# Kernel optimization log

Hardware: AMD Instinct MI355X
Metric: run time of the kernel (lower is better)

Reference implementation:

```python
import jax, jax.numpy as jnp
import numpy as np

N = 100000      # nodes
F_IN = 512      # num_features
H = 256         # hidden
C = 64          # num_classes
E = 3200000     # edges
K = 10          # APPNP propagation steps
ALPHA = 0.1     # teleport probability


def setup_inputs() -> dict:
    key = jax.random.key(0)
    k_x, k_w0, k_w1, k_e = jax.random.split(key, 4)
    x = jax.random.normal(k_x, (N, F_IN), dtype=jnp.float32)
    w0 = jax.random.normal(k_w0, (F_IN, H), dtype=jnp.float32) / np.sqrt(F_IN).astype(np.float32)
    b0 = jnp.zeros((H,), dtype=jnp.float32)
    w1 = jax.random.normal(k_w1, (H, C), dtype=jnp.float32) / np.sqrt(H).astype(np.float32)
    b1 = jnpps = jnp.zeros((C,), dtype=jnp.float32)
    edge_index = jax.random.randint(k_e, (2, E), 0, N, dtype=jnp.int64)
    return {"x": x, "w0": w0, "b0": b0, "w1": w1, "b1": b1, "edge_index": edge_index}


def _appnp(h, edge_index):
    # Add self loops (PyG APPNP default: gcn_norm with self loops).
    loops = jnp.arange(N, dtype=edge_index.dtype)
    src = jnp.concatenate([edge_index[0], loops])
    dst = jnp.concatenate([edge_index[1], loops])
    # Symmetric GCN normalization: D^{-1/2} (A+I) D^{-1/2}
    deg = jax.ops.segment_sum(jnp.ones_like(src, dtype=h.dtype), dst, num_segments=N)
    dinv = jnp.where(deg > 0, jax.lax.rsqrt(deg), 0.0)
    norm = dinv[src] * dinv[dst]  # [E+N]

    def step(xc, _):
        msg = norm[:, None] * xc[src]                      # gather [E+N, C]
        agg = jax.ops.segment_sum(msg, dst, num_segments=N)  # scatter-add [N, C]
        return (1.0 - ALPHA) * agg + ALPHA * h, None

    out, _ = jax.lax.scan(step, h, None, length=K)
    return out


def reference(x, w0, b0, w1, b1, edge_index):
    # eval mode: dropout is identity
    h = jax.nn.relu(x @ w0 + b0)   # [N, H]
    h = h @ w1 + b1                # [N, C]
    z = _appnp(h, edge_index)      # [N, C]
    return jax.nn.log_softmax(z, axis=1)
```

## Files before the change

kernel.cpp:

```cpp
#include <hip/hip_runtime.h>
#include <hip/hip_bf16.h>

#define NN 100000
#define EE 3200000
#define FIN 512
#define HH 256
#define CC 64
#define KSTEPS 10
#define SB 391
#define NBUC 782
#define EPB 16384
#define NEB 196

typedef __attribute__((ext_vector_type(8))) short bf16x8;
typedef __attribute__((ext_vector_type(8))) short s16x8;
typedef __attribute__((ext_vector_type(4))) float f32x4;
typedef unsigned short ushort_t;

__device__ __forceinline__ short f2bf(float f) {
    union { __hip_bfloat16 h; short s; } u;
    u.h = __float2bfloat16(f);
    return u.s;
}

__device__ __forceinline__ void glds16(const void* g, void* l) {
    __builtin_amdgcn_global_load_lds(
        (const __attribute__((address_space(1))) void*)g,
        (__attribute__((address_space(3))) void*)l, 16, 0, 0);
}

__global__ void prep_w(const float* __restrict__ w0, const float* __restrict__ w1,
                       short* __restrict__ w0t, short* __restrict__ w1t) {
    int t = blockIdx.x * blockDim.x + threadIdx.x;
    if (t < FIN * HH) {
        int k = t >> 8, n = t & 255;
        w0t[n * FIN + k] = f2bf(w0[t]);
    } else if (t < FIN * HH + HH * CC) {
        int u = t - FIN * HH;
        int k = u >> 6, n = u & 63;
        w1t[n * HH + k] = f2bf(w1[u]);
    }
}

__global__ __launch_bounds__(256) void x2b_kernel(const float* __restrict__ x,
                                                  ushort_t* __restrict__ xb) {
    const long NTOT = (long)NN * FIN;
    long stride = (long)gridDim.x * 256 * 8;
    for (long i = ((long)blockIdx.x * 256 + threadIdx.x) * 8; i < NTOT; i += stride) {
        float4 a = *(const float4*)(x + i);
        float4 b = *(const float4*)(x + i + 4);
        s16x8 o;
        o[0] = f2bf(a.x); o[1] = f2bf(a.y); o[2] = f2bf(a.z); o[3] = f2bf(a.w);
        o[4] = f2bf(b.x); o[5] = f2bf(b.y); o[6] = f2bf(b.z); o[7] = f2bf(b.w);
        *(s16x8*)(xb + i) = o;
    }
}

__global__ __launch_bounds__(256) void bincnt(const int* __restrict__ ei,
                                              int* __restrict__ bcnt) {
    __shared__ int hb[NBUC];
    int tid = threadIdx.x;
    int base = blockIdx.x * EPB;
    for (int i = tid; i < NBUC; i += 256) hb[i] = 0;
    __syncthreads();
#pragma unroll 4
    for (int i = 0; i < EPB / 256; ++i) {
        int t = base + i * 256 + tid;
        if (t < EE) atomicAdd(&hb[(unsigned)ei[EE + t] >> 7], 1);
    }
    __syncthreads();
    for (int i = tid; i < NBUC; i += 256)
        if (hb[i]) atomicAdd(&bcnt[i], hb[i]);
}

__global__ __launch_bounds__(1024) void bscan(const int* __restrict__ bcnt,
                                              int* __restrict__ eboff) {
    __shared__ int sh[1024];
    int t = threadIdx.x;
    int v = (t < NBUC) ? bcnt[t] : 0;
    sh[t] = v;
    __syncthreads();
    for (int off = 1; off < 1024; off <<= 1) {
        int add = (t >= off) ? sh[t - off] : 0;
        __syncthreads();
        sh[t] += add;
        __syncthreads();
    }
    if (t < NBUC) eboff[t] = sh[t] - v;
}

__global__ __launch_bounds__(256) void binfill(const int* __restrict__ ei,
                                               const int* __restrict__ eboff,
                                               int* __restrict__ bfc,
                                               int* __restrict__ stg) {
    __shared__ int hb[NBUC];
    __shared__ int lb[NBUC];
    int tid = threadIdx.x;
    int base = blockIdx.x * EPB;
    for (int i = tid; i < NBUC; i += 256) hb[i] = 0;
    __syncthreads();
#pragma unroll 4
    for (int i = 0; i < EPB / 256; ++i) {
        int t = base + i * 256 + tid;
        if (t < EE) atomicAdd(&hb[(unsigned)ei[EE + t] >> 7], 1);
    }
    __syncthreads();
    for (int i = tid; i < NBUC; i += 256) {
        int c = hb[i];
        lb[i] = eboff[i] + (c ? atomicAdd(&bfc[i], c) : 0);
        hb[i] = 0;
    }
    __syncthreads();
#pragma unroll 4
    for (int i = 0; i < EPB / 256; ++i) {
        int t = base + i * 256 + tid;
        if (t < EE) {
            int s = ei[t];
            int d = ei[EE + t];
            int b = (unsigned)d >> 7;
            int o = atomicAdd(&hb[b], 1);
            stg[lb[b] + o] = (s << 7) | (d & 127);
        }
    }
}

__global__ __launch_bounds__(256) void bhist(const int* __restrict__ stg,
                                             const int* __restrict__ eboff,
                                             const int* __restrict__ bcnt,
                                             int* __restrict__ cnt) {
    __shared__ int nc[128];
    int b = blockIdx.x, tid = threadIdx.x;
    if (tid < 128) nc[tid] = 0;
    __syncthreads();
    int s0 = eboff[b], n = bcnt[b];
    for (int i = tid; i < n; i += 256) atomicAdd(&nc[stg[s0 + i] & 127], 1);
    __syncthreads();
    int node = b * 128 + tid;
    if (tid < 128 && node < NN) cnt[node] = nc[tid];
}

__global__ __launch_bounds__(256) void deg_kernel(const int* __restrict__ cnt,
                                                  float* __restrict__ dinv,
                                                  float* __restrict__ wco,
                                                  float* __restrict__ sdg,
                                                  int* __restrict__ bsum,
                                                  int* __restrict__ dbc) {
    __shared__ int red[256];
    __shared__ int h[64];
    int tid = threadIdx.x;
    if (tid < 64) h[tid] = 0;
    int i = blockIdx.x * 256 + tid;
    int d = 0, bin = 0;
    if (i < NN) {
        int c = cnt[i];
        d = c + 1;
        bin = min(c, 63);
        float fd = (float)d;
        dinv[i] = rsqrtf(fd);
        wco[i] = 0.9f / fd;
        sdg[i] = sqrtf(fd);
    }
    red[tid] = d;
    __syncthreads();
    if (i < NN) atomicAdd(&h[bin], 1);
    for (int off = 128; off > 0; off >>= 1) {
        if (tid < off) red[tid] += red[tid + off];
        __syncthreads();
    }
    if (tid == 0) bsum[blockIdx.x] = red[0];
    if (tid < 64 && h[tid]) atomicAdd(&dbc[tid], h[tid]);
}

__global__ __launch_bounds__(512) void scanb_kernel(const int* __restrict__ bsum,
                                                    int* __restrict__ boff,
                                                    const int* __restrict__ dbc,
                                                    int* __restrict__ dboff) {
    __shared__ int sh[512];
    int t = threadIdx.x;
    int v = (t < SB) ? bsum[t] : 0;
    sh[t] = v;
    __syncthreads();
    for (int off = 1; off < 512; off <<= 1) {
        int add = (t >= off) ? sh[t - off] : 0;
        __syncthreads();
        sh[t] += add;
        __syncthreads();
    }
    if (t < SB) boff[t] = sh[t] - v;
    __syncthreads();
    int v2 = (t < 64) ? dbc[t] : 0;
    __syncthreads();
    if (t < 64) sh[t] = v2;
    __syncthreads();
    for (int off = 1; off < 64; off <<= 1) {
        int add = (t >= off && t < 64) ? sh[t - off] : 0;
        __syncthreads();
        if (t < 64) sh[t] += add;
        __syncthreads();
    }
    if (t < 64) dboff[t] = sh[t] - v2;
}

__global__ __launch_bounds__(256) void rp_kernel(const int* __restrict__ cnt,
                                                 const int* __restrict__ boff,
                                                 int* __restrict__ rp) {
    __shared__ int sh[256];
    int i = blockIdx.x * 256 + threadIdx.x;
    int d = (i < NN) ? cnt[i] + 1 : 0;
    sh[threadIdx.x] = d;
    __syncthreads();
    for (int off = 1; off < 256; off <<= 1) {
        int add = (threadIdx.x >= off) ? sh[threadIdx.x - off] : 0;
        __syncthreads();
        sh[threadIdx.x] += add;
        __syncthreads();
    }
    int incl = sh[threadIdx.x];
    if (i < NN) rp[i] = boff[blockIdx.x] + incl - d;
    if (i == NN - 1) rp[NN] = boff[blockIdx.x] + incl;
}

__global__ __launch_bounds__(256) void bfill2(const int* __restrict__ stg,
                                              const int* __restrict__ eboff,
                                              const int* __restrict__ bcnt,
                                              const int* __restrict__ rp,
                                              int* __restrict__ eds) {
    __shared__ int nfc[128];
    __shared__ int rpl[129];
    int b = blockIdx.x, tid = threadIdx.x;
    int nodes = min(128, NN - b * 128);
    if (tid < 128) nfc[tid] = 0;
    if (tid <= 128) rpl[tid] = rp[min(b * 128 + tid, NN)];
    __syncthreads();
    int s0 = eboff[b], n = bcnt[b];
    for (int i = tid; i < n; i += 256) {
        int e = stg[s0 + i];
        int loc = e & 127;
        int o = atomicAdd(&nfc[loc], 1);
        eds[rpl[loc] + o] = e >> 7;
    }
    __syncthreads();
    if (tid < nodes) eds[rpl[tid + 1] - 1] = b * 128 + tid;
}

__global__ __launch_bounds__(256) void dperm(const int* __restrict__ cnt,
                                             const int* __restrict__ dboff,
                                             int* __restrict__ dfc,
                                             int* __restrict__ perm) {
    __shared__ int h[64];
    __shared__ int base[64];
    int tid = threadIdx.x;
    int i = blockIdx.x * 256 + tid;
    if (tid < 64) h[tid] = 0;
    __syncthreads();
    int bin = 0, r = 0;
    bool ok = i < NN;
    if (ok) {
        bin = min(cnt[i], 63);
        r = atomicAdd(&h[bin], 1);
    }
    __syncthreads();
    if (tid < 64) {
        int c = h[tid];
        base[tid] = dboff[tid] + (c ? atomicAdd(&dfc[tid], c) : 0);
    }
    __syncthreads();
    if (ok) perm[base[bin] + r] = i;
}

__global__ __launch_bounds__(256) void gemm1(const ushort_t* __restrict__ xb,
                                             const short* __restrict__ w0t,
                                             const float* __restrict__ b0,
                                             short* __restrict__ h0) {
    __shared__ __align__(16) short As[2][128 * 64];
    __shared__ __align__(16) short Bs[2][128 * 64];
    const int tid = threadIdx.x;
    const int lane = tid & 63;
    const int wid = tid >> 6;
    const int wm = wid >> 1, wn = wid & 1;
    const int bn0 = blockIdx.x * 128;
    const long row0 = (long)blockIdx.y * 128;
    const int rl = lane >> 3;
    const int gko = (lane & 7) ^ rl;

    auto stage = [&](int kt, int buf) {
#pragma unroll
        for (int j = 0; j < 4; ++j) {
            int blk = wid * 4 + j;
            const ushort_t* g = xb + (row0 + blk * 8 + rl) * FIN + kt * 64 + gko * 8;
            glds16(g, &As[buf][blk * 512]);
        }
#pragma unroll
        for (int j = 0; j < 4; ++j) {
            int blk = wid * 4 + j;
            const short* g = w0t + (size_t)(bn0 + blk * 8 + rl) * FIN + kt * 64 + gko * 8;
            glds16(g, &Bs[buf][blk * 512]);
        }
    };

    f32x4 acc[4][4] = {};
    stage(0, 0);
    __syncthreads();
    for (int kt = 0; kt < FIN / 64; ++kt) {
        int cur = kt & 1;
        if (kt < FIN / 64 - 1) stage(kt + 1, cur ^ 1);
#pragma unroll
        for (int ks = 0; ks < 2; ++ks) {
            int ko = ks * 4 + (lane >> 4);
            int slot = ko ^ (lane & 7);
            bf16x8 af[4], bfr[4];
#pragma unroll
            for (int i = 0; i < 4; ++i) {
                int row = wm * 64 + i * 16 + (lane & 15);
                af[i] = *(const bf16x8*)(&As[cur][(row * 8 + slot) * 8]);
            }
#pragma unroll
            for (int j = 0; j < 4; ++j) {
                int col = wn * 64 + j * 16 + (lane & 15);
                bfr[j] = *(const bf16x8*)(&Bs[cur][(col * 8 + slot) * 8]);
            }
#pragma unroll
            for (int i = 0; i < 4; ++i)
#pragma unroll
                for (int j = 0; j < 4; ++j)
                    acc[i][j] = __builtin_amdgcn_mfma_f32_16x16x32_bf16(af[i], bfr[j], acc[i][j], 0, 0, 0);
        }
        __syncthreads();
    }
#pragma unroll
    for (int j = 0; j < 4; ++j) {
        int gcol = bn0 + wn * 64 + j * 16 + (lane & 15);
        float bias = b0[gcol];
#pragma unroll
        for (int i = 0; i < 4; ++i)
#pragma unroll
            for (int q = 0; q < 4; ++q) {
                long grow = row0 + wm * 64 + i * 16 + (lane >> 4) * 4 + q;
                float v = acc[i][j][q] + bias;
                if (v < 0.f) v = 0.f;
                h0[grow * HH + gcol] = f2bf(v);
            }
    }
}

__global__ __launch_bounds__(256) void gemm2(const short* __restrict__ h0,
                                             const short* __restrict__ w1t,
                                             const float* __restrict__ b1,
                                             const float* __restrict__ dinv,
                                             ushort_t* __restrict__ hvb,
                                             ushort_t* __restrict__ v0) {
    __shared__ __align__(16) short As[2][128 * 64];
    __shared__ __align__(16) short Bs[2][64 * 64];
    const int tid = threadIdx.x;
    const int lane = tid & 63;
    const int wid = tid >> 6;
    const int wm = wid >> 1, wn = wid & 1;
    const long row0 = (long)blockIdx.x * 128;
    const int rl = lane >> 3;
    const int gko = (lane & 7) ^ rl;

    auto stage = [&](int kt, int buf) {
#pragma unroll
        for (int j = 0; j < 4; ++j) {
            int blk = wid * 4 + j;
            const short* g = h0 + (row0 + blk * 8 + rl) * HH + kt * 64 + gko * 8;
            glds16(g, &As[buf][blk * 512]);
        }
#pragma unroll
        for (int j = 0; j < 2; ++j) {
            int blk = wid * 2 + j;
            const short* g = w1t + (size_t)(blk * 8 + rl) * HH + kt * 64 + gko * 8;
            glds16(g, &Bs[buf][blk * 512]);
        }
    };

    f32x4 acc[4][2] = {};
    stage(0, 0);
    __syncthreads();
    for (int kt = 0; kt < HH / 64; ++kt) {
        int cur = kt & 1;
        if (kt < HH / 64 - 1) stage(kt + 1, cur ^ 1);
#pragma unroll
        for (int ks = 0; ks < 2; ++ks) {
            int ko = ks * 4 + (lane >> 4);
            int slot = ko ^ (lane & 7);
            bf16x8 af[4], bfr[2];
#pragma unroll
            for (int i = 0; i < 4; ++i) {
                int row = wm * 64 + i * 16 + (lane & 15);
                af[i] = *(const bf16x8*)(&As[cur][(row * 8 + slot) * 8]);
            }
#pragma unroll
            for (int j = 0; j < 2; ++j) {
                int col = wn * 32 + j * 16 + (lane & 15);
                bfr[j] = *(const bf16x8*)(&Bs[cur][(col * 8 + slot) * 8]);
            }
#pragma unroll
            for (int i = 0; i < 4; ++i)
#pragma unroll
                for (int j = 0; j < 2; ++j)
                    acc[i][j] = __builtin_amdgcn_mfma_f32_16x16x32_bf16(af[i], bfr[j], acc[i][j], 0, 0, 0);
        }
        __syncthreads();
    }
#pragma unroll
    for (int i = 0; i < 4; ++i)
#pragma unroll
        for (int j = 0; j < 2; ++j) {
            int col = wn * 32 + j * 16 + (lane & 15);
            float bias = b1[col];
#pragma unroll
            for (int q = 0; q < 4; ++q) {
                long grow = row0 + wm * 64 + i * 16 + (lane >> 4) * 4 + q;
                if (grow < NN) {
                    float hval = acc[i][j][q] + bias;
                    float dv = dinv[grow];
                    hvb[grow * CC + col] = (ushort_t)f2bf(0.1f * dv * hval);
                    v0[grow * CC + col] = (ushort_t)f2bf(dv * hval);
                }
            }
        }
}

__device__ __forceinline__ void gath(float a[8], const ushort_t* __restrict__ vin,
                                     int src, int l) {
    const int4 r = *(const int4*)(vin + ((size_t)src << 6) + (l << 3));
    a[0] += __int_as_float(r.x << 16);
    a[1] += __int_as_float(r.x & 0xffff0000);
    a[2] += __int_as_float(r.y << 16);
    a[3] += __int_as_float(r.y & 0xffff0000);
    a[4] += __int_as_float(r.z << 16);
    a[5] += __int_as_float(r.z & 0xffff0000);
    a[6] += __int_as_float(r.w << 16);
    a[7] += __int_as_float(r.w & 0xffff0000);
}

template <int LAST>
__global__ __launch_bounds__(256) void prop(const ushort_t* __restrict__ vin,
                                            const ushort_t* __restrict__ hvb,
                                            const float* __restrict__ wco,
                                            const float* __restrict__ sdg,
                                            ushort_t* __restrict__ vout,
                                            float* __restrict__ zout,
                                            const int* __restrict__ rp,
                                            const int* __restrict__ eds,
                                            const int* __restrict__ perm) {
    int g = perm[blockIdx.x * 32 + (threadIdx.x >> 3)];
    int l = threadIdx.x & 7;
    int beg = rp[g], end = rp[g + 1];
    float a0[8] = {}, a1[8] = {}, a2[8] = {}, a3[8] = {};
    int e = beg;
    int head = (beg + 3) & ~3;
    if (head > end) head = end;
    for (; e < head; ++e) gath(a0, vin, eds[e], l);
    for (; e + 3 < end; e += 4) {
        int4 ee = *(const int4*)(eds + e);
        gath(a0, vin, ee.x, l);
        gath(a1, vin, ee.y, l);
        gath(a2, vin, ee.z, l);
        gath(a3, vin, ee.w, l);
    }
    for (; e < end; ++e) gath(a1, vin, eds[e], l);

    float w = wco[g];
    const int4 hb = *(const int4*)(hvb + ((size_t)g << 6) + (l << 3));
    float tv[8];
    tv[0] = __int_as_float(hb.x << 16);
    tv[1] = __int_as_float(hb.x & 0xffff0000);
    tv[2] = __int_as_float(hb.y << 16);
    tv[3] = __int_as_float(hb.y & 0xffff0000);
    tv[4] = __int_as_float(hb.z << 16);
    tv[5] = __int_as_float(hb.z & 0xffff0000);
    tv[6] = __int_as_float(hb.w << 16);
    tv[7] = __int_as_float(hb.w & 0xffff0000);
    float r[8];
#pragma unroll
    for (int c = 0; c < 8; ++c)
        r[c] = w * ((a0[c] + a1[c]) + (a2[c] + a3[c])) + tv[c];
    if (!LAST) {
        s16x8 o;
#pragma unroll
        for (int c = 0; c < 8; ++c) o[c] = f2bf(r[c]);
        *(s16x8*)(vout + ((size_t)g << 6) + (l << 3)) = o;
    } else {
        float sd = sdg[g];
#pragma unroll
        for (int c = 0; c < 8; ++c) r[c] *= sd;
        float m = r[0];
#pragma unroll
        for (int c = 1; c < 8; ++c) m = fmaxf(m, r[c]);
#pragma unroll
        for (int off = 1; off < 8; off <<= 1) m = fmaxf(m, __shfl_xor(m, off));
        float s = 0.f;
#pragma unroll
        for (int c = 0; c < 8; ++c) s += expf(r[c] - m);
#pragma unroll
        for (int off = 1; off < 8; off <<= 1) s += __shfl_xor(s, off);
        float ls = m + logf(s);
        f32x4 o0, o1;
#pragma unroll
        for (int c = 0; c < 4; ++c) { o0[c] = r[c] - ls; o1[c] = r[c + 4] - ls; }
        *(f32x4*)(zout + ((size_t)g << 6) + (l << 3)) = o0;
        *(f32x4*)(zout + ((size_t)g << 6) + (l << 3) + 4) = o1;
    }
}

extern "C" void kernel_launch(void* const* d_in, const int* in_sizes, int n_in,
                              void* d_out, int out_size, void* d_ws, size_t ws_size,
                              hipStream_t stream) {
    const float* x  = (const float*)d_in[0];
    const float* w0 = (const float*)d_in[1];
    const float* b0 = (const float*)d_in[2];
    const float* w1 = (const float*)d_in[3];
    const float* b1 = (const float*)d_in[4];
    const int*   ei = (const int*)d_in[5];

    char* ws = (char*)d_ws;
    size_t off = 0;
    auto take = [&](size_t n) { size_t r = off; off += (n + 255) & ~(size_t)255; return r; };
    size_t o_h0    = take((size_t)100096 * HH * 2);
    size_t o_vA    = take((size_t)NN * CC * 2);
    size_t o_hv    = take((size_t)NN * CC * 2);
    size_t o_ed    = take((size_t)(EE + NN) * 4);
    size_t o_rp    = take((size_t)(NN + 1) * 4);
    size_t o_cnt   = take((size_t)NN * 4);
    size_t o_dinv  = take((size_t)NN * 4);
    size_t o_wco   = take((size_t)NN * 4);
    size_t o_sdg   = take((size_t)NN * 4);
    size_t o_perm  = take((size_t)NN * 4);
    size_t o_w0t   = take((size_t)HH * FIN * 2);
    size_t o_w1t   = take((size_t)CC * HH * 2);
    size_t o_bs    = take((size_t)SB * 4);
    size_t o_bo    = take((size_t)SB * 4);
    size_t o_eboff = take((size_t)NBUC * 4);
    size_t o_dboff = take((size_t)64 * 4);
    size_t o_z     = take((size_t)(NBUC + NBUC + 64 + 64) * 4);
    size_t o_xb    = take((size_t)100096 * FIN * 2);

    short*    h0    = (short*)(ws + o_h0);
    ushort_t* vA    = (ushort_t*)(ws + o_vA);
    ushort_t* vB    = (ushort_t*)(ws + o_h0);
    ushort_t* hvb   = (ushort_t*)(ws + o_hv);
    int*      stg   = (int*)(ws + o_hv);
    int*      eds   = (int*)(ws + o_ed);
    int*      rp    = (int*)(ws + o_rp);
    int*      cnt   = (int*)(ws + o_cnt);
    float*    dinv  = (float*)(ws + o_dinv);
    float*    wco   = (float*)(ws + o_wco);
    float*    sdg   = (float*)(ws + o_sdg);
    int*      perm  = (int*)(ws + o_perm);
    short*    w0t   = (short*)(ws + o_w0t);
    short*    w1t   = (short*)(ws + o_w1t);
    int*      bs    = (int*)(ws + o_bs);
    int*      bo    = (int*)(ws + o_bo);
    int*      eboff = (int*)(ws + o_eboff);
    int*      dboff = (int*)(ws + o_dboff);
    int*      bcnt  = (int*)(ws + o_z);
    int*      bfc   = bcnt + NBUC;
    int*      dbc   = bfc + NBUC;
    int*      dfc   = dbc + 64;
    ushort_t* xb    = (ushort_t*)(ws + o_xb);
    float*    zout  = (float*)d_out;

    prep_w<<<(FIN * HH + HH * CC + 255) / 256, 256, 0, stream>>>(w0, w1, w0t, w1t);
    hipMemsetAsync(ws + o_z, 0, (size_t)(NBUC + NBUC + 64 + 64) * 4, stream);

    bincnt<<<NEB, 256, 0, stream>>>(ei, bcnt);
    bscan<<<1, 1024, 0, stream>>>(bcnt, eboff);
    binfill<<<NEB, 256, 0, stream>>>(ei, eboff, bfc, stg);
    bhist<<<NBUC, 256, 0, stream>>>(stg, eboff, bcnt, cnt);
    deg_kernel<<<SB, 256, 0, stream>>>(cnt, dinv, wco, sdg, bs, dbc);
    scanb_kernel<<<1, 512, 0, stream>>>(bs, bo, dbc, dboff);
    rp_kernel<<<SB, 256, 0, stream>>>(cnt, bo, rp);
    bfill2<<<NBUC, 256, 0, stream>>>(stg, eboff, bcnt, rp, eds);
    dperm<<<SB, 256, 0, stream>>>(cnt, dboff, dfc, perm);

    x2b_kernel<<<2048, 256, 0, stream>>>(x, xb);
    gemm1<<<dim3(2, 782), 256, 0, stream>>>(xb, w0t, b0, h0);
    gemm2<<<782, 256, 0, stream>>>(h0, w1t, b1, dinv, hvb, vA);

    const ushort_t* in = vA;
    for (int k = 0; k < KSTEPS; ++k) {
        if (k == KSTEPS - 1) {
            prop<1><<<NN / 32, 256, 0, stream>>>(in, hvb, wco, sdg, nullptr, zout, rp, eds, perm);
        } else {
            ushort_t* o = (k & 1) ? vA : vB;
            prop<0><<<NN / 32, 256, 0, stream>>>(in, hvb, wco, sdg, o, nullptr, rp, eds, perm);
            in = o;
        }
    }
}
```

Before: 930.9 us.

## Split node features into column slices to shrink propagation gather working set

Stores propagated node features in four column slices of 16 bf16 values each (slice-major layout) and runs each propagation step over a 2D grid where blockIdx.y picks the slice. Each gather then touches a 3.2 MB slice instead of the full 12.8 MB feature table, which is meant to improve L2 cache hit rates for random source reads. Edge index and self-term loads and output stores become nontemporal. The log-softmax moves out of the last propagation step into a separate kernel, since a row is now spread across slices. The cost is that edge indices and row pointers are read four times, each gather is only 4 bytes per lane, and there is one extra launch.

```diff
diff --git a/kernel.cpp b/kernel.cpp
--- a/kernel.cpp
+++ b/kernel.cpp
@@ -11,10 +11,14 @@
 #define NBUC 782
 #define EPB 16384
 #define NEB 196
+#define NSL 4
+#define SLC 16
 
 typedef __attribute__((ext_vector_type(8))) short bf16x8;
 typedef __attribute__((ext_vector_type(8))) short s16x8;
 typedef __attribute__((ext_vector_type(4))) float f32x4;
+typedef __attribute__((ext_vector_type(2))) float f32x2;
+typedef __attribute__((ext_vector_type(4))) int i32x4;
 typedef unsigned short ushort_t;
 
 __device__ __forceinline__ short f2bf(float f) {
@@ -409,100 +413,89 @@
         for (int j = 0; j < 2; ++j) {
             int col = wn * 32 + j * 16 + (lane & 15);
             float bias = b1[col];
+            int sl = col >> 4, cw = col & 15;
 #pragma unroll
             for (int q = 0; q < 4; ++q) {
                 long grow = row0 + wm * 64 + i * 16 + (lane >> 4) * 4 + q;
                 if (grow < NN) {
                     float hval = acc[i][j][q] + bias;
                     float dv = dinv[grow];
-                    hvb[grow * CC + col] = (ushort_t)f2bf(0.1f * dv * hval);
-                    v0[grow * CC + col] = (ushort_t)f2bf(dv * hval);
+                    size_t idx = (size_t)sl * NN * SLC + grow * SLC + cw;
+                    hvb[idx] = (ushort_t)f2bf(0.1f * dv * hval);
+                    v0[idx] = (ushort_t)f2bf(dv * hval);
                 }
             }
         }
 }
 
-__device__ __forceinline__ void gath(float a[8], const ushort_t* __restrict__ vin,
-                                     int src, int l) {
-    const int4 r = *(const int4*)(vin + ((size_t)src << 6) + (l << 3));
-    a[0] += __int_as_float(r.x << 16);
-    a[1] += __int_as_float(r.x & 0xffff0000);
-    a[2] += __int_as_float(r.y << 16);
-    a[3] += __int_as_float(r.y & 0xffff0000);
-    a[4] += __int_as_float(r.z << 16);
-    a[5] += __int_as_float(r.z & 0xffff0000);
-    a[6] += __int_as_float(r.w << 16);
-    a[7] += __int_as_float(r.w & 0xffff0000);
+__device__ __forceinline__ void gath16(float& ax, float& ay,
+                                       const ushort_t* __restrict__ vs, int src, int l) {
+    int r = *(const int*)(vs + ((size_t)src << 4) + (l << 1));
+    ax += __int_as_float(r << 16);
+    ay += __int_as_float(r & 0xffff0000);
 }
 
 template <int LAST>
-__global__ __launch_bounds__(256) void prop(const ushort_t* __restrict__ vin,
-                                            const ushort_t* __restrict__ hvb,
-                                            const float* __restrict__ wco,
-                                            const float* __restrict__ sdg,
-                                            ushort_t* __restrict__ vout,
-                                            float* __restrict__ zout,
-                                            const int* __restrict__ rp,
-                                            const int* __restrict__ eds,
-                                            const int* __restrict__ perm) {
+__global__ __launch_bounds__(256) void prop16(const ushort_t* __restrict__ vin,
+                                              const ushort_t* __restrict__ hvb,
+                                              const float* __restrict__ wco,
+                                              const float* __restrict__ sdg,
+                                              ushort_t* __restrict__ vout,
+                                              float* __restrict__ zout,
+                                              const int* __restrict__ rp,
+                                              const int* __restrict__ eds,
+                                              const int* __restrict__ perm) {
+    const int slice = blockIdx.y;
+    const ushort_t* vs = vin + (size_t)slice * NN * SLC;
     int g = perm[blockIdx.x * 32 + (threadIdx.x >> 3)];
     int l = threadIdx.x & 7;
     int beg = rp[g], end = rp[g + 1];
-    float a0[8] = {}, a1[8] = {}, a2[8] = {}, a3[8] = {};
+    float ax0 = 0.f, ay0 = 0.f, ax1 = 0.f, ay1 = 0.f;
+    float ax2 = 0.f, ay2 = 0.f, ax3 = 0.f, ay3 = 0.f;
     int e = beg;
     int head = (beg + 3) & ~3;
     if (head > end) head = end;
-    for (; e < head; ++e) gath(a0, vin, eds[e], l);
+    for (; e < head; ++e) gath16(ax0, ay0, vs, eds[e], l);
     for (; e + 3 < end; e += 4) {
-        int4 ee = *(const int4*)(eds + e);
-        gath(a0, vin, ee.x, l);
-        gath(a1, vin, ee.y, l);
-        gath(a2, vin, ee.z, l);
-        gath(a3, vin, ee.w, l);
-    }
-    for (; e < end; ++e) gath(a1, vin, eds[e], l);
+        i32x4 ee = __builtin_nontemporal_load((const i32x4*)(eds + e));
+        gath16(ax0, ay0, vs, ee[0], l);
+        gath16(ax1, ay1, vs, ee[1], l);
+        gath16(ax2, ay2, vs, ee[2], l);
+        gath16(ax3, ay3, vs, ee[3], l);
+    }
+    for (; e < end; ++e) gath16(ax1, ay1, vs, eds[e], l);
 
     float w = wco[g];
-    const int4 hb = *(const int4*)(hvb + ((size_t)g << 6) + (l << 3));
-    float tv[8];
-    tv[0] = __int_as_float(hb.x << 16);
-    tv[1] = __int_as_float(hb.x & 0xffff0000);
-    tv[2] = __int_as_float(hb.y << 16);
-    tv[3] = __int_as_float(hb.y & 0xffff0000);
-    tv[4] = __int_as_float(hb.z << 16);
-    tv[5] = __int_as_float(hb.z & 0xffff0000);
-    tv[6] = __int_as_float(hb.w << 16);
-    tv[7] = __int_as_float(hb.w & 0xffff0000);
-    float r[8];
-#pragma unroll
-    for (int c = 0; c < 8; ++c)
-        r[c] = w * ((a0[c] + a1[c]) + (a2[c] + a3[c])) + tv[c];
+    int hb = __builtin_nontemporal_load(
+        (const int*)(hvb + (size_t)slice * NN * SLC + ((size_t)g << 4) + (l << 1)));
+    float r0 = w * ((ax0 + ax1) + (ax2 + ax3)) + __int_as_float(hb << 16);
+    float r1 = w * ((ay0 + ay1) + (ay2 + ay3)) + __int_as_float(hb & 0xffff0000);
     if (!LAST) {
-        s16x8 o;
-#pragma unroll
-        for (int c = 0; c < 8; ++c) o[c] = f2bf(r[c]);
-        *(s16x8*)(vout + ((size_t)g << 6) + (l << 3)) = o;
+        int o = ((int)(unsigned short)f2bf(r0)) | (((int)(unsigned short)f2bf(r1)) << 16);
+        __builtin_nontemporal_store(
+            o, (int*)(vout + (size_t)slice * NN * SLC + ((size_t)g << 4) + (l << 1)));
     } else {
         float sd = sdg[g];
-#pragma unroll
-        for (int c = 0; c < 8; ++c) r[c] *= sd;
-        float m = r[0];
-#pragma unroll
-        for (int c = 1; c < 8; ++c) m = fmaxf(m, r[c]);
-#pragma unroll
-        for (int off = 1; off < 8; off <<= 1) m = fmaxf(m, __shfl_xor(m, off));
-        float s = 0.f;
-#pragma unroll
-        for (int c = 0; c < 8; ++c) s += expf(r[c] - m);
-#pragma unroll
-        for (int off = 1; off < 8; off <<= 1) s += __shfl_xor(s, off);
-        float ls = m + logf(s);
-        f32x4 o0, o1;
-#pragma unroll
-        for (int c = 0; c < 4; ++c) { o0[c] = r[c] - ls; o1[c] = r[c + 4] - ls; }
-        *(f32x4*)(zout + ((size_t)g << 6) + (l << 3)) = o0;
-        *(f32x4*)(zout + ((size_t)g << 6) + (l << 3) + 4) = o1;
-    }
+        f32x2 o;
+        o[0] = r0 * sd;
+        o[1] = r1 * sd;
+        *(f32x2*)(zout + ((size_t)g << 6) + slice * SLC + (l << 1)) = o;
+    }
+}
+
+__global__ __launch_bounds__(256) void lsm(float* __restrict__ z) {
+    int node = blockIdx.x * 4 + (threadIdx.x >> 6);
+    if (node >= NN) return;
+    int lane = threadIdx.x & 63;
+    float v = z[((size_t)node << 6) + lane];
+    float m = v;
+#pragma unroll
+    for (int off = 32; off > 0; off >>= 1) m = fmaxf(m, __shfl_xor(m, off));
+    float e = expf(v - m);
+    float s = e;
+#pragma unroll
+    for (int off = 32; off > 0; off >>= 1) s += __shfl_xor(s, off);
+    z[((size_t)node << 6) + lane] = v - m - logf(s);
 }
 
 extern "C" void kernel_launch(void* const* d_in, const int* in_sizes, int n_in,
@@ -582,11 +575,12 @@
     const ushort_t* in = vA;
     for (int k = 0; k < KSTEPS; ++k) {
         if (k == KSTEPS - 1) {
-            prop<1><<<NN / 32, 256, 0, stream>>>(in, hvb, wco, sdg, nullptr, zout, rp, eds, perm);
+            prop16<1><<<dim3(NN / 32, NSL), 256, 0, stream>>>(in, hvb, wco, sdg, nullptr, zout, rp, eds, perm);
         } else {
             ushort_t* o = (k & 1) ? vA : vB;
-            prop<0><<<NN / 32, 256, 0, stream>>>(in, hvb, wco, sdg, o, nullptr, rp, eds, perm);
+            prop16<0><<<dim3(NN / 32, NSL), 256, 0, stream>>>(in, hvb, wco, sdg, o, nullptr, rp, eds, perm);
             in = o;
         }
     }
-}
+    lsm<<<(NN + 3) / 4, 256, 0, stream>>>(zout);
+}
```

Measured after the change: 1.928 ms. +107.1%, slower.

## Fuse CSR build kernels into one per-bucket pass and use nontemporal loads in prop

Applied to the files above, without the earlier changes.

Merges the degree histogram, degree-derived scalars, row-pointer scan and edge fill into one bucket_finish kernel. It computes row pointers locally, as bucket edge offset plus bucket index times 128 plus a local scan, so the global block-sum scan and two launches go away. It also reads stg only twice in one kernel instead of across two. Separately, the prop kernel now uses nontemporal loads for edge indices and hvb and nontemporal stores for outputs, to reduce cache pollution for the gathered features. The nontemporal output store could hurt, because that output is re-read by the next step.

```diff
diff --git a/kernel.cpp b/kernel.cpp
--- a/kernel.cpp
+++ b/kernel.cpp
@@ -15,6 +15,7 @@
 typedef __attribute__((ext_vector_type(8))) short bf16x8;
 typedef __attribute__((ext_vector_type(8))) short s16x8;
 typedef __attribute__((ext_vector_type(4))) float f32x4;
+typedef __attribute__((ext_vector_type(4))) int i32x4;
 typedef unsigned short ushort_t;
 
 __device__ __forceinline__ short f2bf(float f) {
@@ -124,123 +125,73 @@
     }
 }
 
-__global__ __launch_bounds__(256) void bhist(const int* __restrict__ stg,
-                                             const int* __restrict__ eboff,
-                                             const int* __restrict__ bcnt,
-                                             int* __restrict__ cnt) {
+__global__ __launch_bounds__(256) void bucket_finish(
+    const int* __restrict__ stg, const int* __restrict__ eboff,
+    const int* __restrict__ bcnt,
+    int* __restrict__ cnt, float* __restrict__ dinv, float* __restrict__ wco,
+    float* __restrict__ sdg, int* __restrict__ rp, int* __restrict__ eds,
+    int* __restrict__ dbc) {
     __shared__ int nc[128];
+    __shared__ int sc[128];
+    __shared__ int lrp[128];
+    __shared__ int nfc[128];
+    __shared__ int h64[64];
     int b = blockIdx.x, tid = threadIdx.x;
-    if (tid < 128) nc[tid] = 0;
+    int nodes = min(128, NN - b * 128);
+    if (tid < 128) { nc[tid] = 0; nfc[tid] = 0; }
+    if (tid < 64) h64[tid] = 0;
     __syncthreads();
     int s0 = eboff[b], n = bcnt[b];
     for (int i = tid; i < n; i += 256) atomicAdd(&nc[stg[s0 + i] & 127], 1);
     __syncthreads();
-    int node = b * 128 + tid;
-    if (tid < 128 && node < NN) cnt[node] = nc[tid];
-}
-
-__global__ __launch_bounds__(256) void deg_kernel(const int* __restrict__ cnt,
-                                                  float* __restrict__ dinv,
-                                                  float* __restrict__ wco,
-                                                  float* __restrict__ sdg,
-                                                  int* __restrict__ bsum,
-                                                  int* __restrict__ dbc) {
-    __shared__ int red[256];
-    __shared__ int h[64];
-    int tid = threadIdx.x;
-    if (tid < 64) h[tid] = 0;
-    int i = blockIdx.x * 256 + tid;
-    int d = 0, bin = 0;
-    if (i < NN) {
-        int c = cnt[i];
-        d = c + 1;
-        bin = min(c, 63);
-        float fd = (float)d;
-        dinv[i] = rsqrtf(fd);
-        wco[i] = 0.9f / fd;
-        sdg[i] = sqrtf(fd);
-    }
-    red[tid] = d;
-    __syncthreads();
-    if (i < NN) atomicAdd(&h[bin], 1);
-    for (int off = 128; off > 0; off >>= 1) {
-        if (tid < off) red[tid] += red[tid + off];
-        __syncthreads();
-    }
-    if (tid == 0) bsum[blockIdx.x] = red[0];
-    if (tid < 64 && h[tid]) atomicAdd(&dbc[tid], h[tid]);
-}
-
-__global__ __launch_bounds__(512) void scanb_kernel(const int* __restrict__ bsum,
-                                                    int* __restrict__ boff,
-                                                    const int* __restrict__ dbc,
-                                                    int* __restrict__ dboff) {
-    __shared__ int sh[512];
-    int t = threadIdx.x;
-    int v = (t < SB) ? bsum[t] : 0;
-    sh[t] = v;
-    __syncthreads();
-    for (int off = 1; off < 512; off <<= 1) {
-        int add = (t >= off) ? sh[t - off] : 0;
-        __syncthreads();
-        sh[t] += add;
-        __syncthreads();
-    }
-    if (t < SB) boff[t] = sh[t] - v;
-    __syncthreads();
-    int v2 = (t < 64) ? dbc[t] : 0;
-    __syncthreads();
-    if (t < 64) sh[t] = v2;
-    __syncthreads();
-    for (int off = 1; off < 64; off <<= 1) {
-        int add = (t >= off && t < 64) ? sh[t - off] : 0;
-        __syncthreads();
-        if (t < 64) sh[t] += add;
-        __syncthreads();
-    }
-    if (t < 64) dboff[t] = sh[t] - v2;
-}
-
-__global__ __launch_bounds__(256) void rp_kernel(const int* __restrict__ cnt,
-                                                 const int* __restrict__ boff,
-                                                 int* __restrict__ rp) {
-    __shared__ int sh[256];
-    int i = blockIdx.x * 256 + threadIdx.x;
-    int d = (i < NN) ? cnt[i] + 1 : 0;
-    sh[threadIdx.x] = d;
-    __syncthreads();
-    for (int off = 1; off < 256; off <<= 1) {
-        int add = (threadIdx.x >= off) ? sh[threadIdx.x - off] : 0;
-        __syncthreads();
-        sh[threadIdx.x] += add;
-        __syncthreads();
-    }
-    int incl = sh[threadIdx.x];
-    if (i < NN) rp[i] = boff[blockIdx.x] + incl - d;
-    if (i == NN - 1) rp[NN] = boff[blockIdx.x] + incl;
-}
-
-__global__ __launch_bounds__(256) void bfill2(const int* __restrict__ stg,
-                                              const int* __restrict__ eboff,
-                                              const int* __restrict__ bcnt,
-                                              const int* __restrict__ rp,
-                                              int* __restrict__ eds) {
-    __shared__ int nfc[128];
-    __shared__ int rpl[129];
-    int b = blockIdx.x, tid = threadIdx.x;
-    int nodes = min(128, NN - b * 128);
-    if (tid < 128) nfc[tid] = 0;
-    if (tid <= 128) rpl[tid] = rp[min(b * 128 + tid, NN)];
-    __syncthreads();
-    int s0 = eboff[b], n = bcnt[b];
+    if (tid < 128) sc[tid] = (tid < nodes) ? nc[tid] + 1 : 0;
+    __syncthreads();
+    for (int off = 1; off < 128; off <<= 1) {
+        int add = (tid < 128 && tid >= off) ? sc[tid - off] : 0;
+        __syncthreads();
+        if (tid < 128) sc[tid] += add;
+        __syncthreads();
+    }
+    int base = eboff[b] + b * 128;
+    if (tid < nodes) {
+        int node = b * 128 + tid;
+        int c = nc[tid];
+        int excl = base + sc[tid] - (c + 1);
+        lrp[tid] = excl;
+        rp[node] = excl;
+        cnt[node] = c;
+        float fd = (float)(c + 1);
+        dinv[node] = rsqrtf(fd);
+        wco[node] = 0.9f / fd;
+        sdg[node] = sqrtf(fd);
+        atomicAdd(&h64[min(c, 63)], 1);
+    }
+    if (b == NBUC - 1 && tid == 0) rp[NN] = base + n + nodes;
+    __syncthreads();
+    if (tid < 64 && h64[tid]) atomicAdd(&dbc[tid], h64[tid]);
     for (int i = tid; i < n; i += 256) {
         int e = stg[s0 + i];
         int loc = e & 127;
         int o = atomicAdd(&nfc[loc], 1);
-        eds[rpl[loc] + o] = e >> 7;
-    }
-    __syncthreads();
-    if (tid < nodes) eds[rpl[tid + 1] - 1] = b * 128 + tid;
+        eds[lrp[loc] + o] = e >> 7;
+    }
+    __syncthreads();
+    if (tid < nodes) eds[lrp[tid] + nc[tid]] = b * 128 + tid;
+}
+
+__global__ void dscan(const int* __restrict__ dbc, int* __restrict__ dboff) {
+    __shared__ int sh[64];
+    int t = threadIdx.x;
+    int v = dbc[t];
+    sh[t] = v;
+    __syncthreads();
+    for (int off = 1; off < 64; off <<= 1) {
+        int add = (t >= off) ? sh[t - off] : 0;
+        __syncthreads();
+        sh[t] += add;
+        __syncthreads();
+    }
+    dboff[t] = sh[t] - v;
 }
 
 __global__ __launch_bounds__(256) void dperm(const int* __restrict__ cnt,
@@ -454,25 +405,26 @@
     if (head > end) head = end;
     for (; e < head; ++e) gath(a0, vin, eds[e], l);
     for (; e + 3 < end; e += 4) {
-        int4 ee = *(const int4*)(eds + e);
-        gath(a0, vin, ee.x, l);
-        gath(a1, vin, ee.y, l);
-        gath(a2, vin, ee.z, l);
-        gath(a3, vin, ee.w, l);
+        i32x4 ee = __builtin_nontemporal_load((const i32x4*)(eds + e));
+        gath(a0, vin, ee[0], l);
+        gath(a1, vin, ee[1], l);
+        gath(a2, vin, ee[2], l);
+        gath(a3, vin, ee[3], l);
     }
     for (; e < end; ++e) gath(a1, vin, eds[e], l);
 
     float w = wco[g];
-    const int4 hb = *(const int4*)(hvb + ((size_t)g << 6) + (l << 3));
+    i32x4 hb = __builtin_nontemporal_load(
+        (const i32x4*)(hvb + ((size_t)g << 6) + (l << 3)));
     float tv[8];
-    tv[0] = __int_as_float(hb.x << 16);
-    tv[1] = __int_as_float(hb.x & 0xffff0000);
-    tv[2] = __int_as_float(hb.y << 16);
-    tv[3] = __int_as_float(hb.y & 0xffff0000);
-    tv[4] = __int_as_float(hb.z << 16);
-    tv[5] = __int_as_float(hb.z & 0xffff0000);
-    tv[6] = __int_as_float(hb.w << 16);
-    tv[7] = __int_as_float(hb.w & 0xffff0000);
+    tv[0] = __int_as_float(hb[0] << 16);
+    tv[1] = __int_as_float(hb[0] & 0xffff0000);
+    tv[2] = __int_as_float(hb[1] << 16);
+    tv[3] = __int_as_float(hb[1] & 0xffff0000);
+    tv[4] = __int_as_float(hb[2] << 16);
+    tv[5] = __int_as_float(hb[2] & 0xffff0000);
+    tv[6] = __int_as_float(hb[3] << 16);
+    tv[7] = __int_as_float(hb[3] & 0xffff0000);
     float r[8];
 #pragma unroll
     for (int c = 0; c < 8; ++c)
@@ -481,7 +433,7 @@
         s16x8 o;
 #pragma unroll
         for (int c = 0; c < 8; ++c) o[c] = f2bf(r[c]);
-        *(s16x8*)(vout + ((size_t)g << 6) + (l << 3)) = o;
+        __builtin_nontemporal_store(o, (s16x8*)(vout + ((size_t)g << 6) + (l << 3)));
     } else {
         float sd = sdg[g];
 #pragma unroll
@@ -530,8 +482,6 @@
     size_t o_perm  = take((size_t)NN * 4);
     size_t o_w0t   = take((size_t)HH * FIN * 2);
     size_t o_w1t   = take((size_t)CC * HH * 2);
-    size_t o_bs    = take((size_t)SB * 4);
-    size_t o_bo    = take((size_t)SB * 4);
     size_t o_eboff = take((size_t)NBUC * 4);
     size_t o_dboff = take((size_t)64 * 4);
     size_t o_z     = take((size_t)(NBUC + NBUC + 64 + 64) * 4);
@@ -551,8 +501,6 @@
     int*      perm  = (int*)(ws + o_perm);
     short*    w0t   = (short*)(ws + o_w0t);
     short*    w1t   = (short*)(ws + o_w1t);
-    int*      bs    = (int*)(ws + o_bs);
-    int*      bo    = (int*)(ws + o_bo);
     int*      eboff = (int*)(ws + o_eboff);
     int*      dboff = (int*)(ws + o_dboff);
     int*      bcnt  = (int*)(ws + o_z);
@@ -568,11 +516,8 @@
     bincnt<<<NEB, 256, 0, stream>>>(ei, bcnt);
     bscan<<<1, 1024, 0, stream>>>(bcnt, eboff);
     binfill<<<NEB, 256, 0, stream>>>(ei, eboff, bfc, stg);
-    bhist<<<NBUC, 256, 0, stream>>>(stg, eboff, bcnt, cnt);
-    deg_kernel<<<SB, 256, 0, stream>>>(cnt, dinv, wco, sdg, bs, dbc);
-    scanb_kernel<<<1, 512, 0, stream>>>(bs, bo, dbc, dboff);
-    rp_kernel<<<SB, 256, 0, stream>>>(cnt, bo, rp);
-    bfill2<<<NBUC, 256, 0, stream>>>(stg, eboff, bcnt, rp, eds);
+    bucket_finish<<<NBUC, 256, 0, stream>>>(stg, eboff, bcnt, cnt, dinv, wco, sdg, rp, eds, dbc);
+    dscan<<<1, 64, 0, stream>>>(dbc, dboff);
     dperm<<<SB, 256, 0, stream>>>(cnt, dboff, dfc, perm);
 
     x2b_kernel<<<2048, 256, 0, stream>>>(x, xb);
```

New measurement: 1.020 ms. 9.6% more time.
